# Performance work log

Measured on AMD Instinct MI355X. Metric: run time of the kernel, lower is better.

## Reference

```python
import jax, jax.numpy as jnp
import numpy as np

NUM_EXPERTS = 8
D_MODEL = 768
D_FF = 4 * D_MODEL


def setup_inputs() -> dict:
    key = jax.random.key(0)
    ks = jax.random.split(key, 7)
    s = 0.02
    x = jax.random.normal(ks[0], (2, 1024, D_MODEL), dtype=jnp.float32)
    router_w = jax.random.normal(ks[1], (D_MODEL, NUM_EXPERTS), dtype=jnp.float32) * s
    router_b = jnp.zeros((NUM_EXPERTS,), dtype=jnp.float32)
    w1 = jax.random.normal(ks[2], (NUM_EXPERTS, D_MODEL, D_FF), dtype=jnp.float32) * s
    b1 = jnp.zeros((NUM_EXPERTS, D_FF), dtype=jnp.float32)
    w2 = jax.random.normal(ks[3], (NUM_EXPERTS, D_FF, D_MODEL), dtype=jnp.float32) * s
    b2 = jnp.zeros((NUM_EXPERTS, D_MODEL), dtype=jnp.float32)
    return {"x": x, "router_w": router_w, "router_b": router_b,
            "w1": w1, "b1": b1, "w2": w2, "b2": b2}


def reference(x, router_w, router_b, w1, b1, w2, b2):
    B, S, D = x.shape
    x_flat = x.reshape(-1, D)                      # [T, D]
    logits = x_flat @ router_w + router_b          # [T, E]
    probs = jax.nn.softmax(logits, axis=-1)
    expert_idx = jnp.argmax(probs, axis=-1)        # [T] int, top-1 routing
    onehot = jax.nn.one_hot(expert_idx, NUM_EXPERTS, dtype=x.dtype)  # [T, E]

    # Per-expert FFN; combine via top-1 one-hot (output is NOT scaled by prob,
    # matching the original). Dropout is eval-mode identity.
    out = jnp.zeros_like(x_flat)
    for e in range(NUM_EXPERTS):
        h = jax.nn.relu(x_flat @ w1[e] + b1[e])    # [T, D_FF]
        y = h @ w2[e] + b2[e]                      # [T, D]
        out = out + onehot[:, e:e + 1] * y
    outputs = out.reshape(B, S, D)

    # Load-balance loss: MSE between empirical expert usage and uniform.
    usage = jnp.bincount(expert_idx, length=NUM_EXPERTS).astype(jnp.float32)
    usage = usage / usage.sum()
    uniform = jnp.full((NUM_EXPERTS,), 1.0 / NUM_EXPERTS, dtype=jnp.float32)
    load_balance_loss = jnp.mean((usage - uniform) ** 2)
    return outputs, load_balance_loss
```

## Files before the change

### kernel.cpp

```cpp
#include <hip/hip_runtime.h>
#include <hip/hip_bf16.h>

#define NTOK 2048
#define DMODEL 768
#define DFF 3072
#define NEXP 8
#define MAXTILE 40

typedef short bf16x8 __attribute__((ext_vector_type(8)));
typedef float f32x4 __attribute__((ext_vector_type(4)));

typedef __attribute__((address_space(1))) const char GCHAR;
typedef __attribute__((address_space(3))) char LCHAR;
#define GL16(g, l) __builtin_amdgcn_global_load_lds((GCHAR*)(g), (LCHAR*)(l), 16, 0, 0)

template <int K, int N>
__device__ void transpose_tile(const float* __restrict__ W, __hip_bfloat16* __restrict__ WT,
                               int e, int k0, int n0, float* T) {
  const int t = threadIdx.x;
  {
    const int kr = t >> 4;
    const int nc = (t & 15) * 4;
    const float* src = W + ((size_t)e * K + k0) * N + n0;
#pragma unroll
    for (int i = 0; i < 4; i++) {
      float4 v = *(const float4*)(src + (size_t)(kr + i * 16) * N + nc);
      T[(kr + i * 16) * 65 + nc + 0] = v.x;
      T[(kr + i * 16) * 65 + nc + 1] = v.y;
      T[(kr + i * 16) * 65 + nc + 2] = v.z;
      T[(kr + i * 16) * 65 + nc + 3] = v.w;
    }
  }
  __syncthreads();
  {
    const int n = t >> 2;
    const int kq = (t & 3) * 16;
    __align__(16) __hip_bfloat16 u[16];
#pragma unroll
    for (int j = 0; j < 16; j++) u[j] = __float2bfloat16(T[(kq + j) * 65 + n]);
    __hip_bfloat16* dst = WT + ((size_t)e * N + n0 + n) * K + k0 + kq;
    *(int4*)dst = *(const int4*)&u[0];
    *(int4*)(dst + 8) = *(const int4*)&u[8];
  }
}

__global__ __launch_bounds__(256) void k_router_t1(
    const float* __restrict__ x, const float* __restrict__ rw,
    const float* __restrict__ rb, __hip_bfloat16* __restrict__ xbf,
    int* __restrict__ eidx, int* __restrict__ cnt,
    const float* __restrict__ w1, __hip_bfloat16* __restrict__ wT1) {
  __shared__ float T[64 * 65];
  if (blockIdx.x >= 512) {
    int tb = blockIdx.x - 512;
    int n_i = tb % (DFF / 64);
    int k_i = (tb / (DFF / 64)) % (DMODEL / 64);
    int e = tb / ((DFF / 64) * (DMODEL / 64));
    transpose_tile<DMODEL, DFF>(w1, wT1, e, k_i * 64, n_i * 64, T);
    return;
  }
  int tok = (blockIdx.x * blockDim.x + threadIdx.x) >> 6;
  int lane = threadIdx.x & 63;
  if (tok >= NTOK) return;
  const float* xr = x + (size_t)tok * DMODEL;
  double acc[NEXP];
#pragma unroll
  for (int e = 0; e < NEXP; e++) acc[e] = 0.0;
  for (int d0 = 0; d0 < DMODEL; d0 += 64) {
    float v = xr[d0 + lane];
    xbf[(size_t)tok * DMODEL + d0 + lane] = __float2bfloat16(v);
    const float* wrow = rw + (size_t)(d0 + lane) * NEXP;
#pragma unroll
    for (int e = 0; e < NEXP; e++) acc[e] += (double)v * (double)wrow[e];
  }
#pragma unroll
  for (int e = 0; e < NEXP; e++) {
    double a = acc[e];
#pragma unroll
    for (int s = 32; s > 0; s >>= 1) a += __shfl_xor(a, s);
    acc[e] = a;
  }
  if (lane == 0) {
    int best = 0;
    double bv = acc[0] + (double)rb[0];
#pragma unroll
    for (int e = 1; e < NEXP; e++) {
      double v = acc[e] + (double)rb[e];
      if (v > bv) { bv = v; best = e; }
    }
    eidx[tok] = best;
    atomicAdd(&cnt[best], 1);
  }
}

__global__ void k_scan(const int* __restrict__ cnt, int* __restrict__ off,
                       int* __restrict__ cur, float* __restrict__ loss,
                       int* __restrict__ tiles, int* __restrict__ ntile) {
  if (threadIdx.x == 0) {
    int s = 0;
    float l = 0.f;
    int nt = 0;
    for (int e = 0; e < NEXP; e++) {
      off[e] = s;
      cur[e] = s;
      for (int m = 0; m < cnt[e]; m += 64) tiles[nt++] = (e << 20) | m;
      s += cnt[e];
      float u = (float)cnt[e] / (float)NTOK - 1.0f / (float)NEXP;
      l += u * u;
    }
    *ntile = nt;
    *loss = l / (float)NEXP;
  }
}

__global__ __launch_bounds__(256) void k_build(const int* __restrict__ eidx,
                                               int* __restrict__ cur,
                                               int* __restrict__ list) {
  int t = blockIdx.x * blockDim.x + threadIdx.x;
  if (t < NTOK) {
    int e = eidx[t];
    int p = atomicAdd(&cur[e], 1);
    list[p] = t;
  }
}

template <int K_TOT, int KCHUNK, int N, int NSPLIT, bool RELU_BF16, bool GATHER_A,
          bool ATOMIC_C, int TK, int TN>
__global__ __launch_bounds__(256) void k_gemm3(
    const __hip_bfloat16* __restrict__ A, const __hip_bfloat16* __restrict__ BT,
    const float* __restrict__ bias, void* __restrict__ Cout,
    const int* __restrict__ cnt, const int* __restrict__ off,
    const int* __restrict__ list, const int* __restrict__ tiles,
    const int* __restrict__ ntile, const float* __restrict__ Tsrc,
    __hip_bfloat16* __restrict__ Tdst) {
  constexpr int NX = N / 128;
  constexpr int W = NX * MAXTILE * NSPLIT;
  __shared__ __align__(16) char smem[49152];

  if constexpr (TK > 0) {
    if (blockIdx.x >= W) {
      int tb = blockIdx.x - W;
      int n_i = tb % (TN / 64);
      int k_i = (tb / (TN / 64)) % (TK / 64);
      int e = tb / ((TN / 64) * (TK / 64));
      transpose_tile<TK, TN>(Tsrc, Tdst, e, k_i * 64, n_i * 64, (float*)smem);
      return;
    }
  }

  int b = blockIdx.x;
  constexpr int q = W / 8, r = W % 8;
  const int xcd = b & 7, ii = b >> 3;
  const int widx = (xcd < r ? xcd * (q + 1) : r * (q + 1) + (xcd - r) * q) + ii;
  const int split = widx % NSPLIT;
  const int rest = widx / NSPLIT;
  const int ti = rest % MAXTILE;
  const int nx = rest / MAXTILE;
  if (ti >= *ntile) return;
  const int tv = tiles[ti];
  const int e = tv >> 20;
  const int m0 = tv & 0xFFFFF;
  const int ce = cnt[e];
  const int oe = off[e];
  const int n0 = nx * 128;
  const int kbase = split * KCHUNK;

  const int tid = threadIdx.x;
  const int lane = tid & 63;
  const int w = tid >> 6;
  const int wr = (w >> 1) * 32;
  const int wc = (w & 1) * 64;
  const int fr = lane & 15;
  const int hi = lane >> 4;

  const int srow = tid >> 3;
  const int cch = (tid & 7) ^ (srow & 7);

  const __hip_bfloat16* ga[2];
#pragma unroll
  for (int j = 0; j < 2; j++) {
    int mr = m0 + j * 32 + srow;
    int src;
    if (GATHER_A) {
      src = list[oe + (mr < ce ? mr : 0)];
    } else {
      int p = oe + mr;
      src = p < NTOK ? p : NTOK - 1;
    }
    ga[j] = A + (size_t)src * K_TOT + kbase + cch * 8;
  }
  const __hip_bfloat16* gb[4];
#pragma unroll
  for (int j = 0; j < 4; j++) {
    int nr = n0 + j * 32 + srow;
    gb[j] = BT + ((size_t)e * N + nr) * K_TOT + kbase + cch * 8;
  }

  char* lA = smem + tid * 16;
  char* lB = smem + 16384 + tid * 16;

  f32x4 acc[2][4] = {};
  constexpr int NT = KCHUNK / 64;

#define STAGE(buf, kc)                                  \
  do {                                                  \
    GL16(ga[0] + (kc), lA + (buf)*8192 + 0 * 4096);     \
    GL16(ga[1] + (kc), lA + (buf)*8192 + 1 * 4096);     \
    GL16(gb[0] + (kc), lB + (buf)*16384 + 0 * 4096);    \
    GL16(gb[1] + (kc), lB + (buf)*16384 + 1 * 4096);    \
    GL16(gb[2] + (kc), lB + (buf)*16384 + 2 * 4096);    \
    GL16(gb[3] + (kc), lB + (buf)*16384 + 3 * 4096);    \
  } while (0)

  STAGE(0, 0);
  int curb = 0;
#pragma unroll 1
  for (int t = 0; t < NT; ++t) {
    if (t + 1 < NT) {
      STAGE(curb ^ 1, (t + 1) * 64);
      asm volatile("s_waitcnt vmcnt(6)" ::: "memory");
    } else {
      asm volatile("s_waitcnt vmcnt(0)" ::: "memory");
    }
    __builtin_amdgcn_s_barrier();
    {
      bf16x8 fa[2][2], fb[4][2];
      const int swz = fr & 7;
#pragma unroll
      for (int mf = 0; mf < 2; mf++)
#pragma unroll
        for (int ks = 0; ks < 2; ks++)
          fa[mf][ks] = *(const bf16x8*)(lA - tid * 16 + curb * 8192 +
                                        (wr + mf * 16 + fr) * 128 +
                                        (((ks * 4 + hi) ^ swz) * 16));
#pragma unroll
      for (int nf = 0; nf < 4; nf++)
#pragma unroll
        for (int ks = 0; ks < 2; ks++)
          fb[nf][ks] = *(const bf16x8*)(lB - tid * 16 + curb * 16384 +
                                        (wc + nf * 16 + fr) * 128 +
                                        (((ks * 4 + hi) ^ swz) * 16));
#pragma unroll
      for (int ks = 0; ks < 2; ks++)
#pragma unroll
        for (int mf = 0; mf < 2; mf++)
#pragma unroll
          for (int nf = 0; nf < 4; nf++)
            acc[mf][nf] = __builtin_amdgcn_mfma_f32_16x16x32_bf16(fa[mf][ks], fb[nf][ks],
                                                                  acc[mf][nf], 0, 0, 0);
    }
    __builtin_amdgcn_s_barrier();
    asm volatile("" ::: "memory");
    curb ^= 1;
  }
#undef STAGE

#pragma unroll
  for (int mf = 0; mf < 2; mf++) {
#pragma unroll
    for (int jj = 0; jj < 4; jj++) {
      const int mloc = m0 + wr + mf * 16 + hi * 4 + jj;
      if (mloc >= ce) continue;
      if (RELU_BF16) {
        __hip_bfloat16* C = (__hip_bfloat16*)Cout;
        size_t row = (size_t)(oe + mloc) * N;
        const float* bi = bias + (size_t)e * N;
#pragma unroll
        for (int nf = 0; nf < 4; nf++) {
          int nn = n0 + wc + nf * 16 + fr;
          float v = acc[mf][nf][jj] + bi[nn];
          C[row + nn] = __float2bfloat16(v > 0.f ? v : 0.f);
        }
      } else {
        float* C = (float*)Cout;
        int tok = list[oe + mloc];
        size_t row = (size_t)tok * N;
        const float* bi = bias + (size_t)e * N;
#pragma unroll
        for (int nf = 0; nf < 4; nf++) {
          int nn = n0 + wc + nf * 16 + fr;
          float v = acc[mf][nf][jj] + (split == 0 ? bi[nn] : 0.f);
          if (ATOMIC_C)
            atomicAdd(&C[row + nn], v);
          else
            C[row + nn] = v;
        }
      }
    }
  }
}

template <int K, int N, bool RELU_BF16, bool GATHER_A, bool SCATTER_C>
__global__ __launch_bounds__(256) void k_gemm(
    const __hip_bfloat16* __restrict__ A, const float* __restrict__ Bw,
    const float* __restrict__ bias, void* __restrict__ Cout,
    const int* __restrict__ cnt, const int* __restrict__ off,
    const int* __restrict__ list) {
  const int e = blockIdx.z;
  const int ce = cnt[e];
  const int m0 = blockIdx.y * 128;
  if (m0 >= ce) return;
  const int oe = off[e];
  const int n0 = blockIdx.x * 128;

  __shared__ __hip_bfloat16 Asm[128][32];
  __shared__ __hip_bfloat16 Bsm[128][32];

  const int tid = threadIdx.x;
  const int ra = tid >> 1;
  const int ha = (tid & 1) * 16;
  size_t arow;
  {
    int mr = m0 + ra;
    int src;
    if (GATHER_A) {
      src = (mr < ce) ? list[oe + mr] : list[oe];
    } else {
      int p = oe + mr;
      src = (p < NTOK) ? p : (NTOK - 1);
    }
    arow = (size_t)src * K;
  }
  const int rbk = tid >> 3;
  const int nb = (tid & 7) * 16;
  const float* bsrc0 = Bw + ((size_t)e * K + rbk) * N + n0 + nb;

  const int w = tid >> 6;
  const int lane = tid & 63;
  const int wr = (w >> 1) * 64;
  const int wc = (w & 1) * 64;
  const int fr = lane & 15;
  const int fk = (lane >> 4) * 8;

  f32x4 acc[4][4] = {};

  for (int k0 = 0; k0 < K; k0 += 32) {
    __syncthreads();
    {
      const __hip_bfloat16* s = A + arow + k0 + ha;
      int4 v0 = *(const int4*)(s);
      int4 v1 = *(const int4*)(s + 8);
      *(int4*)(&Asm[ra][ha]) = v0;
      *(int4*)(&Asm[ra][ha + 8]) = v1;
    }
    {
      const float* s = bsrc0 + (size_t)k0 * N;
      float4 f0 = *(const float4*)(s);
      float4 f1 = *(const float4*)(s + 4);
      float4 f2 = *(const float4*)(s + 8);
      float4 f3 = *(const float4*)(s + 12);
      __hip_bfloat16* dst = &Bsm[nb][0] + rbk;
      dst[0 * 32] = __float2bfloat16(f0.x);
      dst[1 * 32] = __float2bfloat16(f0.y);
      dst[2 * 32] = __float2bfloat16(f0.z);
      dst[3 * 32] = __float2bfloat16(f0.w);
      dst[4 * 32] = __float2bfloat16(f1.x);
      dst[5 * 32] = __float2bfloat16(f1.y);
      dst[6 * 32] = __float2bfloat16(f1.z);
      dst[7 * 32] = __float2bfloat16(f1.w);
      dst[8 * 32] = __float2bfloat16(f2.x);
      dst[9 * 32] = __float2bfloat16(f2.y);
      dst[10 * 32] = __float2bfloat16(f2.z);
      dst[11 * 32] = __float2bfloat16(f2.w);
      dst[12 * 32] = __float2bfloat16(f3.x);
      dst[13 * 32] = __float2bfloat16(f3.y);
      dst[14 * 32] = __float2bfloat16(f3.z);
      dst[15 * 32] = __float2bfloat16(f3.w);
    }
    __syncthreads();

    bf16x8 fa[4], fb[4];
#pragma unroll
    for (int mf = 0; mf < 4; mf++) fa[mf] = *(const bf16x8*)(&Asm[wr + mf * 16 + fr][fk]);
#pragma unroll
    for (int nf = 0; nf < 4; nf++) fb[nf] = *(const bf16x8*)(&Bsm[wc + nf * 16 + fr][fk]);
#pragma unroll
    for (int mf = 0; mf < 4; mf++)
#pragma unroll
      for (int nf = 0; nf < 4; nf++)
        acc[mf][nf] = __builtin_amdgcn_mfma_f32_16x16x32_bf16(fa[mf], fb[nf], acc[mf][nf], 0, 0, 0);
  }

#pragma unroll
  for (int mf = 0; mf < 4; mf++) {
#pragma unroll
    for (int j = 0; j < 4; j++) {
      const int mloc = m0 + wr + mf * 16 + (lane >> 4) * 4 + j;
      if (mloc >= ce) continue;
      if (RELU_BF16) {
        __hip_bfloat16* C = (__hip_bfloat16*)Cout;
        size_t row = (size_t)(oe + mloc) * N;
        const float* bi = bias + (size_t)e * N;
#pragma unroll
        for (int nf = 0; nf < 4; nf++) {
          int nn = n0 + wc + nf * 16 + fr;
          float v = acc[mf][nf][j] + bi[nn];
          C[row + nn] = __float2bfloat16(v > 0.f ? v : 0.f);
        }
      } else {
        float* C = (float*)Cout;
        int tok = SCATTER_C ? list[oe + mloc] : (oe + mloc);
        size_t row = (size_t)tok * N;
        const float* bi = bias + (size_t)e * N;
#pragma unroll
        for (int nf = 0; nf < 4; nf++) {
          int nn = n0 + wc + nf * 16 + fr;
          C[row + nn] = acc[mf][nf][j] + bi[nn];
        }
      }
    }
  }
}

extern "C" void kernel_launch(void* const* d_in, const int* in_sizes, int n_in,
                              void* d_out, int out_size, void* d_ws, size_t ws_size,
                              hipStream_t stream) {
  const float* x = (const float*)d_in[0];
  const float* rw = (const float*)d_in[1];
  const float* rb = (const float*)d_in[2];
  const float* w1 = (const float*)d_in[3];
  const float* b1 = (const float*)d_in[4];
  const float* w2 = (const float*)d_in[5];
  const float* b2 = (const float*)d_in[6];
  float* out = (float*)d_out;

  char* ws = (char*)d_ws;
  int* cnt = (int*)(ws + 0);
  int* off = (int*)(ws + 32);
  int* cur = (int*)(ws + 64);
  int* ntile = (int*)(ws + 96);
  int* tiles = (int*)(ws + 128);
  int* eidx = (int*)(ws + 512);
  int* list = (int*)(ws + 8704);
  __hip_bfloat16* xbf = (__hip_bfloat16*)(ws + 65536);
  __hip_bfloat16* h = (__hip_bfloat16*)(ws + 4194304);
  __hip_bfloat16* wT1 = (__hip_bfloat16*)(ws + 20971520);
  __hip_bfloat16* wT2 = (__hip_bfloat16*)(ws + 58720256);

  float* loss = out + (size_t)2 * 1024 * 768;
  const size_t REQ = 58720256ull + 37748736ull;

  (void)hipMemsetAsync(cnt, 0, 96, stream);
  (void)hipMemsetAsync(d_out, 0, (size_t)out_size * sizeof(float), stream);

  if (ws_size >= REQ) {
    const int TBLK = (DMODEL / 64) * (DFF / 64) * NEXP;
    k_router_t1<<<512 + TBLK, 256, 0, stream>>>(x, rw, rb, xbf, eidx, cnt, w1, wT1);
    k_scan<<<1, 64, 0, stream>>>(cnt, off, cur, loss, tiles, ntile);
    k_build<<<8, 256, 0, stream>>>(eidx, cur, list);
    k_gemm3<DMODEL, DMODEL, DFF, 1, true, true, false, DFF, DMODEL>
        <<<(DFF / 128) * MAXTILE + TBLK, 256, 0, stream>>>(
            xbf, wT1, b1, h, cnt, off, list, tiles, ntile, w2, wT2);
    k_gemm3<DFF, DFF / 4, DMODEL, 4, false, false, true, 0, 64>
        <<<(DMODEL / 128) * MAXTILE * 4, 256, 0, stream>>>(
            h, wT2, b2, out, cnt, off, list, tiles, ntile, nullptr, nullptr);
  } else {
    k_router_t1<<<512, 256, 0, stream>>>(x, rw, rb, xbf, eidx, cnt, w1, wT1);
    k_scan<<<1, 64, 0, stream>>>(cnt, off, cur, loss, tiles, ntile);
    k_build<<<8, 256, 0, stream>>>(eidx, cur, list);
    k_gemm<DMODEL, DFF, true, true, false>
        <<<dim3(DFF / 128, 16, NEXP), 256, 0, stream>>>(xbf, w1, b1, h, cnt, off, list);
    k_gemm<DFF, DMODEL, false, false, true>
        <<<dim3(DMODEL / 128, 16, NEXP), 256, 0, stream>>>(h, w2, b2, out, cnt, off, list);
  }
}
```

Baseline: 147.7 us.

## Use 128x128 expert GEMM tiles with K=32 triple-buffered LDS pipeline

Grows the grouped expert GEMM tile from 64x128 to 128x128 rows, so each wave computes a 64x64 block with 16 accumulators. The K step drops from 64 to 32, and LDS becomes three stages with two loads in flight and a new 4-chunk XOR swizzle. The aim is to reuse each loaded weight tile across twice as many tokens, halving weight traffic per token, and to hide load latency better. In exchange there are fewer blocks (24 max tiles instead of 40), more wasted rows in partial expert tiles, and higher register pressure.

Result: slower. 152.4 us (+3.2%).

```diff
diff --git a/kernel.cpp b/kernel.cpp
--- a/kernel.cpp
+++ b/kernel.cpp
@@ -5,7 +5,7 @@
 #define DMODEL 768
 #define DFF 3072
 #define NEXP 8
-#define MAXTILE 40
+#define MAXT 24
 
 typedef short bf16x8 __attribute__((ext_vector_type(8)));
 typedef float f32x4 __attribute__((ext_vector_type(4)));
@@ -102,7 +102,7 @@
     for (int e = 0; e < NEXP; e++) {
       off[e] = s;
       cur[e] = s;
-      for (int m = 0; m < cnt[e]; m += 64) tiles[nt++] = (e << 20) | m;
+      for (int m = 0; m < cnt[e]; m += 128) tiles[nt++] = (e << 20) | m;
       s += cnt[e];
       float u = (float)cnt[e] / (float)NTOK - 1.0f / (float)NEXP;
       l += u * u;
@@ -125,7 +125,7 @@
 
 template <int K_TOT, int KCHUNK, int N, int NSPLIT, bool RELU_BF16, bool GATHER_A,
           bool ATOMIC_C, int TK, int TN>
-__global__ __launch_bounds__(256) void k_gemm3(
+__global__ __launch_bounds__(256) void k_gemm5(
     const __hip_bfloat16* __restrict__ A, const __hip_bfloat16* __restrict__ BT,
     const float* __restrict__ bias, void* __restrict__ Cout,
     const int* __restrict__ cnt, const int* __restrict__ off,
@@ -133,7 +133,7 @@
     const int* __restrict__ ntile, const float* __restrict__ Tsrc,
     __hip_bfloat16* __restrict__ Tdst) {
   constexpr int NX = N / 128;
-  constexpr int W = NX * MAXTILE * NSPLIT;
+  constexpr int W = NX * MAXT * NSPLIT;
   __shared__ __align__(16) char smem[49152];
 
   if constexpr (TK > 0) {
@@ -153,8 +153,8 @@
   const int widx = (xcd < r ? xcd * (q + 1) : r * (q + 1) + (xcd - r) * q) + ii;
   const int split = widx % NSPLIT;
   const int rest = widx / NSPLIT;
-  const int ti = rest % MAXTILE;
-  const int nx = rest / MAXTILE;
+  const int ti = rest % MAXT;
+  const int nx = rest / MAXT;
   if (ti >= *ntile) return;
   const int tv = tiles[ti];
   const int e = tv >> 20;
@@ -167,95 +167,91 @@
   const int tid = threadIdx.x;
   const int lane = tid & 63;
   const int w = tid >> 6;
-  const int wr = (w >> 1) * 32;
+  const int wr = (w >> 1) * 64;
   const int wc = (w & 1) * 64;
   const int fr = lane & 15;
   const int hi = lane >> 4;
 
-  const int srow = tid >> 3;
-  const int cch = (tid & 7) ^ (srow & 7);
+  const int srow = tid >> 2;
+  const int cch = (tid & 3) ^ ((tid >> 3) & 3);
 
   const __hip_bfloat16* ga[2];
 #pragma unroll
   for (int j = 0; j < 2; j++) {
-    int mr = m0 + j * 32 + srow;
+    int mr = m0 + j * 64 + srow;
     int src;
     if (GATHER_A) {
       src = list[oe + (mr < ce ? mr : 0)];
     } else {
-      int p = oe + mr;
-      src = p < NTOK ? p : NTOK - 1;
+      int p2 = oe + mr;
+      src = p2 < NTOK ? p2 : NTOK - 1;
     }
     ga[j] = A + (size_t)src * K_TOT + kbase + cch * 8;
   }
-  const __hip_bfloat16* gb[4];
-#pragma unroll
-  for (int j = 0; j < 4; j++) {
-    int nr = n0 + j * 32 + srow;
+  const __hip_bfloat16* gb[2];
+#pragma unroll
+  for (int j = 0; j < 2; j++) {
+    int nr = n0 + j * 64 + srow;
     gb[j] = BT + ((size_t)e * N + nr) * K_TOT + kbase + cch * 8;
   }
 
   char* lA = smem + tid * 16;
-  char* lB = smem + 16384 + tid * 16;
-
-  f32x4 acc[2][4] = {};
-  constexpr int NT = KCHUNK / 64;
-
-#define STAGE(buf, kc)                                  \
-  do {                                                  \
-    GL16(ga[0] + (kc), lA + (buf)*8192 + 0 * 4096);     \
-    GL16(ga[1] + (kc), lA + (buf)*8192 + 1 * 4096);     \
-    GL16(gb[0] + (kc), lB + (buf)*16384 + 0 * 4096);    \
-    GL16(gb[1] + (kc), lB + (buf)*16384 + 1 * 4096);    \
-    GL16(gb[2] + (kc), lB + (buf)*16384 + 2 * 4096);    \
-    GL16(gb[3] + (kc), lB + (buf)*16384 + 3 * 4096);    \
+
+  f32x4 acc[4][4] = {};
+  constexpr int NT = KCHUNK / 32;
+
+#define STAGE(buf, kc)                                \
+  do {                                                \
+    GL16(ga[0] + (kc), lA + (buf)*16384 + 0);         \
+    GL16(ga[1] + (kc), lA + (buf)*16384 + 4096);      \
+    GL16(gb[0] + (kc), lA + (buf)*16384 + 8192);      \
+    GL16(gb[1] + (kc), lA + (buf)*16384 + 12288);     \
   } while (0)
 
   STAGE(0, 0);
-  int curb = 0;
+  STAGE(1, 32);
+  int cur = 0, sb = 2;
+  const int xr = (fr >> 1) & 3;
 #pragma unroll 1
   for (int t = 0; t < NT; ++t) {
-    if (t + 1 < NT) {
-      STAGE(curb ^ 1, (t + 1) * 64);
-      asm volatile("s_waitcnt vmcnt(6)" ::: "memory");
+    if (t + 2 < NT) {
+      STAGE(sb, (t + 2) * 32);
+      asm volatile("s_waitcnt vmcnt(8)" ::: "memory");
+    } else if (t + 1 < NT) {
+      asm volatile("s_waitcnt vmcnt(4)" ::: "memory");
     } else {
       asm volatile("s_waitcnt vmcnt(0)" ::: "memory");
     }
     __builtin_amdgcn_s_barrier();
     {
-      bf16x8 fa[2][2], fb[4][2];
-      const int swz = fr & 7;
-#pragma unroll
-      for (int mf = 0; mf < 2; mf++)
-#pragma unroll
-        for (int ks = 0; ks < 2; ks++)
-          fa[mf][ks] = *(const bf16x8*)(lA - tid * 16 + curb * 8192 +
-                                        (wr + mf * 16 + fr) * 128 +
-                                        (((ks * 4 + hi) ^ swz) * 16));
-#pragma unroll
-      for (int nf = 0; nf < 4; nf++)
-#pragma unroll
-        for (int ks = 0; ks < 2; ks++)
-          fb[nf][ks] = *(const bf16x8*)(lB - tid * 16 + curb * 16384 +
-                                        (wc + nf * 16 + fr) * 128 +
-                                        (((ks * 4 + hi) ^ swz) * 16));
-#pragma unroll
-      for (int ks = 0; ks < 2; ks++)
-#pragma unroll
-        for (int mf = 0; mf < 2; mf++)
-#pragma unroll
-          for (int nf = 0; nf < 4; nf++)
-            acc[mf][nf] = __builtin_amdgcn_mfma_f32_16x16x32_bf16(fa[mf][ks], fb[nf][ks],
-                                                                  acc[mf][nf], 0, 0, 0);
+      const char* bA = smem + cur * 16384;
+      const char* bB = bA + 8192;
+      bf16x8 fa[4], fb[4];
+#pragma unroll
+      for (int mf = 0; mf < 4; mf++) {
+        const int row = wr + mf * 16 + fr;
+        fa[mf] = *(const bf16x8*)(bA + row * 64 + ((hi ^ xr) * 16));
+      }
+#pragma unroll
+      for (int nf = 0; nf < 4; nf++) {
+        const int row = wc + nf * 16 + fr;
+        fb[nf] = *(const bf16x8*)(bB + row * 64 + ((hi ^ xr) * 16));
+      }
+#pragma unroll
+      for (int mf = 0; mf < 4; mf++)
+#pragma unroll
+        for (int nf = 0; nf < 4; nf++)
+          acc[mf][nf] = __builtin_amdgcn_mfma_f32_16x16x32_bf16(fa[mf], fb[nf],
+                                                                acc[mf][nf], 0, 0, 0);
     }
     __builtin_amdgcn_s_barrier();
-    asm volatile("" ::: "memory");
-    curb ^= 1;
+    cur = (cur == 2) ? 0 : cur + 1;
+    sb = (sb == 2) ? 0 : sb + 1;
   }
 #undef STAGE
 
 #pragma unroll
-  for (int mf = 0; mf < 2; mf++) {
+  for (int mf = 0; mf < 4; mf++) {
 #pragma unroll
     for (int jj = 0; jj < 4; jj++) {
       const int mloc = m0 + wr + mf * 16 + hi * 4 + jj;
@@ -447,11 +443,11 @@
     k_router_t1<<<512 + TBLK, 256, 0, stream>>>(x, rw, rb, xbf, eidx, cnt, w1, wT1);
     k_scan<<<1, 64, 0, stream>>>(cnt, off, cur, loss, tiles, ntile);
     k_build<<<8, 256, 0, stream>>>(eidx, cur, list);
-    k_gemm3<DMODEL, DMODEL, DFF, 1, true, true, false, DFF, DMODEL>
-        <<<(DFF / 128) * MAXTILE + TBLK, 256, 0, stream>>>(
+    k_gemm5<DMODEL, DMODEL, DFF, 1, true, true, false, DFF, DMODEL>
+        <<<(DFF / 128) * MAXT + TBLK, 256, 0, stream>>>(
             xbf, wT1, b1, h, cnt, off, list, tiles, ntile, w2, wT2);
-    k_gemm3<DFF, DFF / 4, DMODEL, 4, false, false, true, 0, 64>
-        <<<(DMODEL / 128) * MAXTILE * 4, 256, 0, stream>>>(
+    k_gemm5<DFF, DFF / 4, DMODEL, 4, false, false, true, 0, 64>
+        <<<(DMODEL / 128) * MAXT * 4, 256, 0, stream>>>(
             h, wT2, b2, out, cnt, off, list, tiles, ntile, nullptr, nullptr);
   } else {
     k_router_t1<<<512, 256, 0, stream>>>(x, rw, rb, xbf, eidx, cnt, w1, wT1);
```
